# Kernel optimization log

Measured on AMD Instinct MI355X. Metric: run time of the kernel, lower is better.

## Reference

```python
import jax, jax.numpy as jnp
import numpy as np
from jax import lax

B, S, C, L = 256, 30, 62, 169   # batch, timesteps, channels(nodes), data_seg
OG, OH = 64, 64                 # out_gcn, out_gru
K1, K2, K3 = 64, 32, 14         # depthwise kernel sizes (169-63-31-13 = 62 = C)


def setup_inputs() -> dict:
    key = jax.random.key(0)
    ks = jax.random.split(key, 26)
    def n(k, shape, s=0.05):
        return jax.random.normal(k, shape, dtype=jnp.float32) * s
    inp = {
        "x": jax.random.normal(ks[0], (B, S, C, L), dtype=jnp.float32),
        "adj": jax.random.normal(ks[1], (C, C), dtype=jnp.float32),
        # depthwise-separable conv 1 (kernel 64)
        "dw1_w": n(ks[2], (C, 1, K1)), "dw1_b": n(ks[3], (C,)),
        "pw1_w": n(ks[4], (C, C, 1)), "pw1_b": n(ks[5], (C,)),
        # depthwise-separable conv 2 (kernel 32)
        "dw2_w": n(ks[6], (C, 1, K2)), "dw2_b": n(ks[7], (C,)),
        "pw2_w": n(ks[8], (C, C, 1)), "pw2_b": n(ks[9], (C,)),
        # depthwise-separable conv 3 (kernel 14)
        "dw3_w": n(ks[10], (C, 1, K3)), "dw3_b": n(ks[11], (C,)),
        "pw3_w": n(ks[12], (C, C, 1)), "pw3_b": n(ks[13], (C,)),
        # GraphConvolution(data_seg, out_gcn): support = x @ W; out = adj @ support + b
        "gcn_w": n(ks[14], (L, OG)), "gcn_b": n(ks[15], (OG,)),
        # GRU-style gate Linears (out_gcn+out_gru -> out_gru), torch layout (out, in)
        "Wr_w": n(ks[16], (OH, OG + OH)), "Wr_b": n(ks[17], (OH,)),
        "Wu_w": n(ks[18], (OH, OG + OH)), "Wu_b": n(ks[19], (OH,)),
        "Wc_w": n(ks[20], (OH, OG + OH)), "Wc_b": n(ks[21], (OH,)),
        # extra learned gate biases b_r/b_u/b_c (init zeros in torch)
        "b_r": jnp.zeros((OH,), jnp.float32),
        "b_u": jnp.zeros((OH,), jnp.float32),
        "b_c": jnp.zeros((OH,), jnp.float32),
    }
    return inp


def _dsconv(x, dw, dwb, pw, pwb):
    # x: (b, c, l); depthwise (groups=c, valid padding) then pointwise 1x1
    dn = ("NCH", "OIH", "NCH")
    y = lax.conv_general_dilated(x, dw, (1,), "VALID", dimension_numbers=dn,
                                 feature_group_count=x.shape[1]) + dwb[None, :, None]
    y = lax.conv_general_dilated(y, pw, (1,), "VALID", dimension_numbers=dn) + pwb[None, :, None]
    return y


def reference(x, adj, dw1_w, dw1_b, pw1_w, pw1_b, dw2_w, dw2_b, pw2_w, pw2_b,
              dw3_w, dw3_b, pw3_w, pw3_b, gcn_w, gcn_b,
              Wr_w, Wr_b, Wu_w, Wu_b, Wc_w, Wc_b, b_r, b_u, b_c):
    b, s, c, l = x.shape
    oh = b_r.shape[0]

    def step(h, xt):            # h: (b*c, oh), xt: (b, c, l)
        d = _dsconv(xt, dw1_w, dw1_b, pw1_w, pw1_b)
        d = _dsconv(d, dw2_w, dw2_b, pw2_w, pw2_b)
        d = _dsconv(d, dw3_w, dw3_b, pw3_w, pw3_b)      # (b, c, c)
        adj_t = jax.nn.sigmoid(d + adj)                  # adaptive adjacency
        support = jnp.einsum("bcl,lf->bcf", xt, gcn_w)
        g = jnp.einsum("bij,bjf->bif", adj_t, support) + gcn_b  # (b, c, og)
        gf = g.reshape(b * c, -1)
        cat = jnp.concatenate([gf, h], axis=-1)
        r = jax.nn.sigmoid(cat @ Wr_w.T + Wr_b + b_r)
        u = jax.nn.sigmoid(cat @ Wu_w.T + Wu_b + b_u)
        cc = jnp.tanh(jnp.concatenate([gf, r * h], axis=-1) @ Wc_w.T + Wc_b + b_c)
        h_new = u * h + (1.0 - u) * cc
        return h_new, None

    h0 = jnp.zeros((b * c, oh), x.dtype)
    xs = jnp.swapaxes(x, 0, 1)          # (s, b, c, l)
    h_last, _ = lax.scan(step, h0, xs)
    return h_last.reshape(b, c, oh)[:, -1, :]   # (b, out_gru)
```

## Files before the change

### kernel.cpp

```cpp
#include <hip/hip_runtime.h>
#include <math.h>

#define BB 256
#define SS 30
#define CC 62
#define LL 169
#define OG 64
#define OH 64
#define KK1 64
#define KK2 32
#define KK3 14
#define FLEN 108

typedef __attribute__((ext_vector_type(8))) short s16x8;
typedef __attribute__((ext_vector_type(4))) float f32x4;

__device__ __forceinline__ unsigned short f2bf(float f) {
    unsigned u = __float_as_uint(f);
    u += 0x7fffu + ((u >> 16) & 1u);
    return (unsigned short)(u >> 16);
}
__device__ __forceinline__ float bflo(unsigned v) { return __uint_as_float(v << 16); }
__device__ __forceinline__ float bfhi(unsigned v) { return __uint_as_float(v & 0xffff0000u); }

__global__ __launch_bounds__(1024) void k_setup1(
        const float* __restrict__ dw1, const float* __restrict__ dw1b,
        const float* __restrict__ pw1, const float* __restrict__ pw1b,
        const float* __restrict__ dw2, const float* __restrict__ dw2b,
        const float* __restrict__ pw2, const float* __restrict__ pw2b,
        const float* __restrict__ dw3, const float* __restrict__ dw3b,
        const float* __restrict__ pw3, const float* __restrict__ pw3b,
        const float* __restrict__ Wr, const float* __restrict__ Wrb, const float* __restrict__ br,
        const float* __restrict__ Wu, const float* __restrict__ Wub, const float* __restrict__ bu,
        const float* __restrict__ Wc, const float* __restrict__ Wcb, const float* __restrict__ bc,
        float* __restrict__ Bmg, float* __restrict__ WtAll,
        float* __restrict__ bias192, float* __restrict__ beff) {
    __shared__ float g23[CC * KK3];
    __shared__ float Am[CC * 45];
    __shared__ float by2[CC], vals[CC];
    int tid = threadIdx.x;

    for (int idx = tid; idx < OG * 192; idx += 1024) {
        int i = idx / 192, q = idx - i * 192;
        int gate = q >> 6, f = q & 63;
        const float* W = gate == 0 ? Wr : (gate == 1 ? Wu : Wc);
        WtAll[idx] = W[f * (OG + OH) + i];
    }
    if (tid < 192) {
        int gate = tid >> 6, f = tid & 63;
        const float* Wb = gate == 0 ? Wrb : (gate == 1 ? Wub : Wcb);
        const float* bb = gate == 0 ? br  : (gate == 1 ? bu  : bc);
        bias192[tid] = Wb[f] + bb[f];
    }

    for (int idx = tid; idx < CC * KK3; idx += 1024) {
        int c1 = idx / KK3, k3 = idx - c1 * KK3;
        float s = 0.f;
        for (int c2 = 0; c2 < CC; ++c2)
            s += pw3[61 * CC + c2] * pw2[c2 * CC + c1] * dw3[c2 * KK3 + k3];
        g23[idx] = s;
    }
    if (tid < CC) {
        int c1 = tid;
        float bz1 = pw1b[c1];
        for (int c0 = 0; c0 < CC; ++c0) bz1 += pw1[c1 * CC + c0] * dw1b[c0];
        float s2 = 0.f;
        for (int k = 0; k < KK2; ++k) s2 += dw2[c1 * KK2 + k];
        by2[c1] = dw2b[c1] + bz1 * s2;
    }
    __syncthreads();

    if (tid < CC) {
        int c2 = tid;
        float bz2 = pw2b[c2];
        for (int c1 = 0; c1 < CC; ++c1) bz2 += pw2[c2 * CC + c1] * by2[c1];
        float s3 = 0.f;
        for (int k = 0; k < KK3; ++k) s3 += dw3[c2 * KK3 + k];
        vals[c2] = pw3[61 * CC + c2] * (dw3b[c2] + bz2 * s3);
    }
    for (int idx = tid; idx < CC * 45; idx += 1024) {
        int c1 = idx / 45, m = idx - c1 * 45;
        int k2lo = max(0, m - (KK3 - 1));
        int k2hi = min(KK2 - 1, m);
        float s = 0.f;
        for (int k2 = k2lo; k2 <= k2hi; ++k2)
            s += dw2[c1 * KK2 + k2] * g23[c1 * KK3 + (m - k2)];
        Am[idx] = s;
    }
    __syncthreads();

    if (tid == 0) {
        float s = pw3b[61];
        for (int c2 = 0; c2 < CC; ++c2) s += vals[c2];
        *beff = s;
    }
    for (int idx = tid; idx < CC * 45; idx += 1024) {
        int c0 = idx / 45, m = idx - c0 * 45;
        float s = 0.f;
        for (int c1 = 0; c1 < CC; ++c1) s += pw1[c1 * CC + c0] * Am[c1 * 45 + m];
        Bmg[idx] = s;
    }
}

__global__ __launch_bounds__(128) void k_setupF(
        const float* __restrict__ Bmg, const float* __restrict__ dw1,
        unsigned short* __restrict__ Ftb) {
    __shared__ float Bl[45];
    int c0 = blockIdx.x;
    int o = threadIdx.x;
    if (c0 < CC && o < 45) Bl[o] = Bmg[c0 * 45 + o];
    __syncthreads();
    if (o >= 112) return;
    float s = 0.f;
    if (c0 < CC && o < FLEN) {
        int mlo = max(0, o - (KK1 - 1));
        int mhi = min(44, o);
        for (int m = mlo; m <= mhi; ++m)
            s += Bl[m] * dw1[c0 * KK1 + (o - m)];
    }
    Ftb[o * 64 + c0] = f2bf(s);
}

__global__ __launch_bounds__(256, 2) void k_main(
        const float* __restrict__ x, const float* __restrict__ adj,
        const unsigned short* __restrict__ Ftb, const float* __restrict__ beff_p,
        float* __restrict__ wxb) {
    __shared__ __align__(16) unsigned short xT[176 * 64];
    __shared__ float dacc[4][64];
    __shared__ float adjt[CC];
    int bt = blockIdx.x;
    int tid = threadIdx.x;
    const uint2* xg2 = (const uint2*)(x + (size_t)bt * (CC * LL));
    unsigned* xTu = (unsigned*)xT;

    uint2 rg[21];
    #pragma unroll
    for (int i = 0; i < 21; ++i) {
        int p = tid + i * 256;
        if (p > 5238) p = 5238;
        rg[i] = xg2[p];
    }
    float be = *beff_p;
    float arow = 0.f;
    if (tid < CC) arow = adj[61 * CC + tid];
    int lane = tid & 63, wid = tid >> 6;
    int col = lane & 15, rb4 = lane >> 4;
    const unsigned short* ap0 = Ftb + ((wid * 16 + col) * 64 + rb4 * 8);
    s16x8 pa0 = *(const s16x8*)ap0;
    s16x8 pa1 = *(const s16x8*)(ap0 + 32);
    __builtin_amdgcn_sched_barrier(0);

    ((float*)dacc)[tid] = 0.f;
    for (int i = tid; i < 169; i += 256) xTu[(i * 32 + 31) ^ ((i & 7) << 2)] = 0;
    for (int i = tid; i < 224; i += 256) {
        int r = 169 + (i >> 5), d = i & 31;
        xTu[(r * 32 + d) ^ ((r & 7) << 2)] = 0;
    }
    #pragma unroll
    for (int i = 0; i < 21; ++i) {
        int p = tid + i * 256;
        if (p > 5238) p = 5238;
        uint2 v = rg[i];
        int i0 = 2 * p;
        int c = i0 / LL;
        int l = i0 - c * LL;
        *(unsigned short*)((char*)xT + ((l * 128 + 2 * c) ^ ((l & 7) << 4))) =
            f2bf(__uint_as_float(v.x));
        int l2 = l + 1, c2 = c;
        if (l2 == LL) { l2 = 0; c2 = c + 1; }
        *(unsigned short*)((char*)xT + ((l2 * 128 + 2 * c2) ^ ((l2 & 7) << 4))) =
            f2bf(__uint_as_float(v.y));
    }
    __syncthreads();

    f32x4 zacc[5];
    #pragma unroll
    for (int d = 0; d < 5; ++d) zacc[d] = (f32x4){0.f, 0.f, 0.f, 0.f};
    int kb = rb4 * 16;
    int xr = (lane & 7) << 4;
    #pragma unroll
    for (int h = 0; h < 2; ++h) {
        int mt = wid + 4 * h;
        if (mt < 7) {
            s16x8 a0, a1;
            if (h == 0) { a0 = pa0; a1 = pa1; }
            else {
                const unsigned short* ap = Ftb + ((mt * 16 + col) * 64 + rb4 * 8);
                a0 = *(const s16x8*)ap;
                a1 = *(const s16x8*)(ap + 32);
            }
            #pragma unroll
            for (int d = 0; d < 5; ++d) {
                int nt = mt + d;
                int bbyte = ((nt * 16 + col) * 128 + kb) ^ xr;
                s16x8 b0 = *(const s16x8*)((const char*)xT + bbyte);
                s16x8 b1 = *(const s16x8*)((const char*)xT + bbyte + 64);
                zacc[d] = __builtin_amdgcn_mfma_f32_16x16x32_bf16(a0, b0, zacc[d], 0, 0, 0);
                zacc[d] = __builtin_amdgcn_mfma_f32_16x16x32_bf16(a1, b1, zacc[d], 0, 0, 0);
            }
        }
    }
    int jc = col - rb4 * 4;
    #pragma unroll
    for (int d = 0; d < 5; ++d) {
        #pragma unroll
        for (int r = 0; r < 4; ++r) {
            int j = 16 * d + jc - r;
            if ((unsigned)j < 62u) atomicAdd(&dacc[rb4][j], zacc[d][r]);
        }
    }
    __syncthreads();

    if (tid < CC) {
        float dv = dacc[0][tid] + dacc[1][tid] + dacc[2][tid] + dacc[3][tid];
        adjt[tid] = 1.f / (1.f + __expf(-(dv + be + arow)));
    }
    __syncthreads();

    if (tid < 176) {
        float s = 0.f;
        if (tid < LL) {
            int xorv = (tid & 7) << 2;
            #pragma unroll
            for (int m = 0; m < 31; ++m) {
                unsigned v = xTu[(tid * 32 + m) ^ xorv];
                s += adjt[2 * m] * bflo(v) + adjt[2 * m + 1] * bfhi(v);
            }
        }
        wxb[(size_t)bt * 176 + tid] = s;
    }
}

__global__ __launch_bounds__(256) void k_g(
        const float* __restrict__ wxb, const float* __restrict__ gcnw,
        const float* __restrict__ gcnb, float* __restrict__ G) {
    int gid = blockIdx.x * 256 + threadIdx.x;
    int bt = gid >> 6, f = gid & 63;
    const float* wr = wxb + (size_t)bt * 176;
    float s = gcnb[f];
    #pragma unroll 13
    for (int l = 0; l < LL; ++l) s += wr[l] * gcnw[l * OG + f];
    G[gid] = s;
}

__global__ __launch_bounds__(256) void k_gates(
        const float* __restrict__ G, const float* __restrict__ WtAll,
        const float* __restrict__ bias192, float* __restrict__ gates) {
    int gid = blockIdx.x * 256 + threadIdx.x;
    int bt = gid / 192, q = gid - bt * 192;
    const float* gr = G + (size_t)bt * 64;
    float s = bias192[q];
    #pragma unroll 16
    for (int i = 0; i < OG; ++i) s += gr[i] * WtAll[i * 192 + q];
    gates[gid] = s;
}

__global__ __launch_bounds__(256) void k_scan(
        const float* __restrict__ gates,
        const float* __restrict__ Wr, const float* __restrict__ Wu, const float* __restrict__ Wc,
        float* __restrict__ out) {
    __shared__ float hl[OH], rhl[OH];
    int b = blockIdx.x;
    int tid = threadIdx.x;
    int f = tid >> 2, q = tid & 3;
    float wr[16], wu[16], wc[16];
    #pragma unroll
    for (int i = 0; i < 16; ++i) {
        int col = OG + q * 16 + i;
        wr[i] = Wr[f * (OG + OH) + col];
        wu[i] = Wu[f * (OG + OH) + col];
        wc[i] = Wc[f * (OG + OH) + col];
    }
    float h = 0.f;
    if (tid < OH) hl[tid] = 0.f;
    __syncthreads();
    for (int t = 0; t < SS; ++t) {
        const float* gp = gates + ((size_t)b * SS + t) * 192;
        float gr = gp[f];
        float gu = gp[64 + f];
        float gc = gp[128 + f];
        float rv = 0.f, uv = 0.f;
        #pragma unroll
        for (int i = 0; i < 16; ++i) {
            float hv = hl[q * 16 + i];
            rv += wr[i] * hv;
            uv += wu[i] * hv;
        }
        rv += __shfl_xor(rv, 1); rv += __shfl_xor(rv, 2);
        uv += __shfl_xor(uv, 1); uv += __shfl_xor(uv, 2);
        float r = 1.f / (1.f + __expf(-(rv + gr)));
        float u = 1.f / (1.f + __expf(-(uv + gu)));
        if (q == 0) rhl[f] = r * h;
        __syncthreads();
        float cv = 0.f;
        #pragma unroll
        for (int i = 0; i < 16; ++i) cv += wc[i] * rhl[q * 16 + i];
        cv += __shfl_xor(cv, 1); cv += __shfl_xor(cv, 2);
        float cc = tanhf(cv + gc);
        if (q == 0) {
            h = u * h + (1.f - u) * cc;
            hl[f] = h;
        }
        __syncthreads();
    }
    if (q == 0) out[b * OH + f] = h;
}

extern "C" void kernel_launch(void* const* d_in, const int* in_sizes, int n_in,
                              void* d_out, int out_size, void* d_ws, size_t ws_size,
                              hipStream_t stream) {
    const float* x    = (const float*)d_in[0];
    const float* adj  = (const float*)d_in[1];
    const float* dw1w = (const float*)d_in[2];
    const float* dw1b = (const float*)d_in[3];
    const float* pw1w = (const float*)d_in[4];
    const float* pw1b = (const float*)d_in[5];
    const float* dw2w = (const float*)d_in[6];
    const float* dw2b = (const float*)d_in[7];
    const float* pw2w = (const float*)d_in[8];
    const float* pw2b = (const float*)d_in[9];
    const float* dw3w = (const float*)d_in[10];
    const float* dw3b = (const float*)d_in[11];
    const float* pw3w = (const float*)d_in[12];
    const float* pw3b = (const float*)d_in[13];
    const float* gcnw = (const float*)d_in[14];
    const float* gcnb = (const float*)d_in[15];
    const float* Wrw  = (const float*)d_in[16];
    const float* Wrb  = (const float*)d_in[17];
    const float* Wuw  = (const float*)d_in[18];
    const float* Wub  = (const float*)d_in[19];
    const float* Wcw  = (const float*)d_in[20];
    const float* Wcb  = (const float*)d_in[21];
    const float* br   = (const float*)d_in[22];
    const float* bu   = (const float*)d_in[23];
    const float* bc   = (const float*)d_in[24];
    float* out = (float*)d_out;

    char* ws = (char*)d_ws;
    unsigned short* Ftb = (unsigned short*)(ws + 0);
    float* WtAll        = (float*)(ws + 14336);
    float* bias192      = (float*)(ws + 63488);
    float* beff         = (float*)(ws + 64256);
    float* Bmg          = (float*)(ws + 64320);
    float* G            = (float*)(ws + 76800);
    float* wxb          = (float*)(ws + 2042880);
    float* gates        = (float*)(ws + 2042880);
    (void)ws_size; (void)in_sizes; (void)n_in; (void)out_size;

    k_setup1<<<1, 1024, 0, stream>>>(dw1w, dw1b, pw1w, pw1b, dw2w, dw2b, pw2w, pw2b,
                                     dw3w, dw3b, pw3w, pw3b,
                                     Wrw, Wrb, br, Wuw, Wub, bu, Wcw, Wcb, bc,
                                     Bmg, WtAll, bias192, beff);
    k_setupF<<<64, 128, 0, stream>>>(Bmg, dw1w, Ftb);
    k_main<<<BB * SS, 256, 0, stream>>>(x, adj, Ftb, beff, wxb);
    k_g<<<(BB * SS * OG) / 256, 256, 0, stream>>>(wxb, gcnw, gcnb, G);
    k_gates<<<(BB * SS * 192) / 256, 256, 0, stream>>>(G, WtAll, bias192, gates);
    k_scan<<<BB, 256, 0, stream>>>(gates, Wrw, Wuw, Wcw, out);
}
```

Measured before the change: 328.0 us.

## Stage x via direct global-to-LDS loads and fuse GCN and gate kernels

k_main now loads the fp32 x tile straight into shared memory with global_load_lds instead of staging it through registers. It then builds the bf16 transposed tile from that LDS copy, and computes the final adjacency-weighted sum in fp32 from the staged copy. The separate k_g and k_gates kernels are merged into one k_gg kernel that keeps G in shared memory for 8 timesteps per block, removing the G round trip through global memory and one launch. In exchange, k_main uses about 41 KB more LDS per block, which may lower occupancy below the requested 2 blocks per CU, and it adds an extra barrier.

```diff
diff --git a/kernel.cpp b/kernel.cpp
--- a/kernel.cpp
+++ b/kernel.cpp
@@ -22,6 +22,12 @@
 }
 __device__ __forceinline__ float bflo(unsigned v) { return __uint_as_float(v << 16); }
 __device__ __forceinline__ float bfhi(unsigned v) { return __uint_as_float(v & 0xffff0000u); }
+
+__device__ __forceinline__ void gload_lds4(const void* g, void* l) {
+    __builtin_amdgcn_global_load_lds(
+        (const __attribute__((address_space(1))) void*)g,
+        (__attribute__((address_space(3))) void*)l, 4, 0, 0);
+}
 
 __global__ __launch_bounds__(1024) void k_setup1(
         const float* __restrict__ dw1, const float* __restrict__ dw1b,
@@ -52,7 +58,6 @@
         const float* bb = gate == 0 ? br  : (gate == 1 ? bu  : bc);
         bias192[tid] = Wb[f] + bb[f];
     }
-
     for (int idx = tid; idx < CC * KK3; idx += 1024) {
         int c1 = idx / KK3, k3 = idx - c1 * KK3;
         float s = 0.f;
@@ -69,7 +74,6 @@
         by2[c1] = dw2b[c1] + bz1 * s2;
     }
     __syncthreads();
-
     if (tid < CC) {
         int c2 = tid;
         float bz2 = pw2b[c2];
@@ -88,7 +92,6 @@
         Am[idx] = s;
     }
     __syncthreads();
-
     if (tid == 0) {
         float s = pw3b[61];
         for (int c2 = 0; c2 < CC; ++c2) s += vals[c2];
@@ -125,51 +128,45 @@
         const float* __restrict__ x, const float* __restrict__ adj,
         const unsigned short* __restrict__ Ftb, const float* __restrict__ beff_p,
         float* __restrict__ wxb) {
+    __shared__ __align__(16) unsigned xf32[10478];
     __shared__ __align__(16) unsigned short xT[176 * 64];
     __shared__ float dacc[4][64];
     __shared__ float adjt[CC];
     int bt = blockIdx.x;
     int tid = threadIdx.x;
-    const uint2* xg2 = (const uint2*)(x + (size_t)bt * (CC * LL));
+    int lane = tid & 63, wid = tid >> 6;
+    const float* xg = x + (size_t)bt * (CC * LL);
     unsigned* xTu = (unsigned*)xT;
 
-    uint2 rg[21];
-    #pragma unroll
-    for (int i = 0; i < 21; ++i) {
-        int p = tid + i * 256;
-        if (p > 5238) p = 5238;
-        rg[i] = xg2[p];
+    #pragma unroll
+    for (int it = 0; it < 41; ++it) {
+        int di = it * 256 + tid;
+        if (di < 10478)
+            gload_lds4((const char*)xg + (size_t)di * 4,
+                       (char*)xf32 + it * 1024 + wid * 256);
     }
     float be = *beff_p;
     float arow = 0.f;
     if (tid < CC) arow = adj[61 * CC + tid];
-    int lane = tid & 63, wid = tid >> 6;
     int col = lane & 15, rb4 = lane >> 4;
     const unsigned short* ap0 = Ftb + ((wid * 16 + col) * 64 + rb4 * 8);
     s16x8 pa0 = *(const s16x8*)ap0;
     s16x8 pa1 = *(const s16x8*)(ap0 + 32);
-    __builtin_amdgcn_sched_barrier(0);
-
     ((float*)dacc)[tid] = 0.f;
     for (int i = tid; i < 169; i += 256) xTu[(i * 32 + 31) ^ ((i & 7) << 2)] = 0;
     for (int i = tid; i < 224; i += 256) {
-        int r = 169 + (i >> 5), d = i & 31;
-        xTu[(r * 32 + d) ^ ((r & 7) << 2)] = 0;
-    }
-    #pragma unroll
-    for (int i = 0; i < 21; ++i) {
-        int p = tid + i * 256;
-        if (p > 5238) p = 5238;
-        uint2 v = rg[i];
-        int i0 = 2 * p;
-        int c = i0 / LL;
-        int l = i0 - c * LL;
-        *(unsigned short*)((char*)xT + ((l * 128 + 2 * c) ^ ((l & 7) << 4))) =
-            f2bf(__uint_as_float(v.x));
-        int l2 = l + 1, c2 = c;
-        if (l2 == LL) { l2 = 0; c2 = c + 1; }
-        *(unsigned short*)((char*)xT + ((l2 * 128 + 2 * c2) ^ ((l2 & 7) << 4))) =
-            f2bf(__uint_as_float(v.y));
+        int r = 169 + (i >> 5), d2 = i & 31;
+        xTu[(r * 32 + d2) ^ ((r & 7) << 2)] = 0;
+    }
+    __syncthreads();
+
+    for (int idx = tid; idx < 31 * 169; idx += 256) {
+        int l = idx / 31, cp = idx - l * 31;
+        unsigned lo = xf32[(2 * cp) * 169 + l];
+        unsigned hi = xf32[(2 * cp + 1) * 169 + l];
+        unsigned v = (unsigned)f2bf(__uint_as_float(lo))
+                   | ((unsigned)f2bf(__uint_as_float(hi)) << 16);
+        xTu[(l * 32 + cp) ^ ((l & 7) << 2)] = v;
     }
     __syncthreads();
 
@@ -220,39 +217,47 @@
     if (tid < 176) {
         float s = 0.f;
         if (tid < LL) {
-            int xorv = (tid & 7) << 2;
-            #pragma unroll
-            for (int m = 0; m < 31; ++m) {
-                unsigned v = xTu[(tid * 32 + m) ^ xorv];
-                s += adjt[2 * m] * bflo(v) + adjt[2 * m + 1] * bfhi(v);
-            }
+            #pragma unroll 2
+            for (int j = 0; j < CC; ++j)
+                s += adjt[j] * __uint_as_float(xf32[j * LL + tid]);
         }
         wxb[(size_t)bt * 176 + tid] = s;
     }
 }
 
-__global__ __launch_bounds__(256) void k_g(
+__global__ __launch_bounds__(256) void k_gg(
         const float* __restrict__ wxb, const float* __restrict__ gcnw,
-        const float* __restrict__ gcnb, float* __restrict__ G) {
-    int gid = blockIdx.x * 256 + threadIdx.x;
-    int bt = gid >> 6, f = gid & 63;
-    const float* wr = wxb + (size_t)bt * 176;
-    float s = gcnb[f];
-    #pragma unroll 13
-    for (int l = 0; l < LL; ++l) s += wr[l] * gcnw[l * OG + f];
-    G[gid] = s;
-}
-
-__global__ __launch_bounds__(256) void k_gates(
-        const float* __restrict__ G, const float* __restrict__ WtAll,
+        const float* __restrict__ gcnb, const float* __restrict__ WtAll,
         const float* __restrict__ bias192, float* __restrict__ gates) {
-    int gid = blockIdx.x * 256 + threadIdx.x;
-    int bt = gid / 192, q = gid - bt * 192;
-    const float* gr = G + (size_t)bt * 64;
-    float s = bias192[q];
-    #pragma unroll 16
-    for (int i = 0; i < OG; ++i) s += gr[i] * WtAll[i * 192 + q];
-    gates[gid] = s;
+    __shared__ float wxl[8 * 176];
+    __shared__ float Gl[8 * 64];
+    int bt0 = blockIdx.x * 8;
+    int tid = threadIdx.x;
+    const float* src = wxb + (size_t)bt0 * 176;
+    for (int i = tid; i < 8 * 176; i += 256) wxl[i] = src[i];
+    __syncthreads();
+    #pragma unroll
+    for (int rep = 0; rep < 2; ++rep) {
+        int i = rep * 256 + tid;
+        int bl = i >> 6, f = i & 63;
+        float s = gcnb[f];
+        const float* wr = wxl + bl * 176;
+        #pragma unroll 13
+        for (int l = 0; l < LL; ++l) s += wr[l] * gcnw[l * OG + f];
+        Gl[i] = s;
+    }
+    __syncthreads();
+    float* gout = gates + (size_t)bt0 * 192;
+    #pragma unroll
+    for (int rep = 0; rep < 6; ++rep) {
+        int i = rep * 256 + tid;
+        int bl = i / 192, q = i - bl * 192;
+        const float* gr = Gl + bl * 64;
+        float s = bias192[q];
+        #pragma unroll 16
+        for (int k = 0; k < OG; ++k) s += gr[k] * WtAll[k * 192 + q];
+        gout[i] = s;
+    }
 }
 
 __global__ __launch_bounds__(256) void k_scan(
@@ -342,9 +347,8 @@
     float* bias192      = (float*)(ws + 63488);
     float* beff         = (float*)(ws + 64256);
     float* Bmg          = (float*)(ws + 64320);
-    float* G            = (float*)(ws + 76800);
-    float* wxb          = (float*)(ws + 2042880);
-    float* gates        = (float*)(ws + 2042880);
+    float* wxb          = (float*)(ws + 76800);
+    float* gates        = (float*)(ws + 5483520);
     (void)ws_size; (void)in_sizes; (void)n_in; (void)out_size;
 
     k_setup1<<<1, 1024, 0, stream>>>(dw1w, dw1b, pw1w, pw1b, dw2w, dw2b, pw2w, pw2b,
@@ -353,7 +357,6 @@
                                      Bmg, WtAll, bias192, beff);
     k_setupF<<<64, 128, 0, stream>>>(Bmg, dw1w, Ftb);
     k_main<<<BB * SS, 256, 0, stream>>>(x, adj, Ftb, beff, wxb);
-    k_g<<<(BB * SS * OG) / 256, 256, 0, stream>>>(wxb, gcnw, gcnb, G);
-    k_gates<<<(BB * SS * 192) / 256, 256, 0, stream>>>(G, WtAll, bias192, gates);
+    k_gg<<<BB * SS / 8, 256, 0, stream>>>(wxb, gcnw, gcnb, WtAll, bias192, gates);
     k_scan<<<BB, 256, 0, stream>>>(gates, Wrw, Wuw, Wcw, out);
 }
```

New measurement: 340.4 us. 3.8% more time.
